# Performance work log

Hardware: AMD Instinct MI355X
Metric: run time of the kernel (lower is better)

Reference implementation:

```python
import jax, jax.numpy as jnp
import numpy as np

B, LQ, LK = 16, 1024, 2048
E, F, A = 512, 256, 512


def setup_inputs() -> dict:
    key = jax.random.key(0)
    ks = jax.random.split(key, 8)
    s_e = 1.0 / np.sqrt(E)
    s_f = 1.0 / np.sqrt(F)
    s_a = 1.0 / np.sqrt(A)
    return {
        "lstm_embeddings": jax.random.normal(ks[0], (B, LQ, E), jnp.float32),
        "optical_flow_features": jax.random.normal(ks[1], (B, LK, F), jnp.float32),
        "Wq": jax.random.normal(ks[2], (E, A), jnp.float32) * s_e,
        "bq": jnp.zeros((A,), jnp.float32),
        "Wk": jax.random.normal(ks[3], (F, A), jnp.float32) * s_f,
        "bk": jnp.zeros((A,), jnp.float32),
        "Wv": jax.random.normal(ks[4], (F, A), jnp.float32) * s_f,
        "bv": jnp.zeros((A,), jnp.float32),
        "Wo": jax.random.normal(ks[5], (A, E), jnp.float32) * s_a,
        "bo": jnp.zeros((E,), jnp.float32),
    }


def reference(lstm_embeddings, optical_flow_features, Wq, bq, Wk, bk, Wv, bv, Wo, bo):
    # Linear projections (x @ W + b), matching nn.Linear with W stored as [in, out]
    q = lstm_embeddings @ Wq + bq            # [B, LQ, A]
    k = optical_flow_features @ Wk + bk      # [B, LK, A]
    v = optical_flow_features @ Wv + bv      # [B, LK, A]
    # NOTE: original module does NOT scale scores by 1/sqrt(A) — stay faithful.
    scores = jnp.einsum("bqa,bka->bqk", q, k)      # [B, LQ, LK]
    weights = jax.nn.softmax(scores, axis=-1)
    context = jnp.einsum("bqk,bka->bqa", weights, v)  # [B, LQ, A]
    return context @ Wo + bo                          # [B, LQ, E]
```

## Files before the change

### kernel.cpp

```cpp
#include <hip/hip_runtime.h>


#define DEV static __device__ __forceinline__

typedef __attribute__((ext_vector_type(8))) short s8v;
typedef __attribute__((ext_vector_type(8))) _Float16 h8v;
typedef __attribute__((ext_vector_type(4))) _Float16 h4v;
typedef __attribute__((ext_vector_type(4))) float f4v;
typedef __attribute__((ext_vector_type(16))) float f16f;
typedef __attribute__((ext_vector_type(4))) float float4v;
typedef unsigned short u16;
typedef unsigned int u32;

constexpr int BB = 16;
constexpr int LQ = 1024;
constexpr int LK = 2048;
constexpr int E = 512;
constexpr int F = 256;

DEV u16 f2bf(float x) {
    u32 u = __builtin_bit_cast(u32, x);
    u += 0x7fff + ((u >> 16) & 1);
    return (u16)(u >> 16);
}
DEV float bf2f(u16 h) { return __builtin_bit_cast(float, (u32)h << 16); }

DEV f4v MF(s8v a, s8v b, f4v c) {
    return __builtin_amdgcn_mfma_f32_16x16x32_bf16(a, b, c, 0, 0, 0);
}
DEV f4v MF16(h8v a, h8v b, f4v c) {
    return __builtin_amdgcn_mfma_f32_16x16x32_f16(a, b, c, 0, 0, 0);
}
DEV f16f MF32(h8v a, h8v b, f16f c) {
    return __builtin_amdgcn_mfma_f32_32x32x16_f16(a, b, c, 0, 0, 0);
}

DEV void gll16(const _Float16* g, _Float16* l) {
    __builtin_amdgcn_global_load_lds(
        (const __attribute__((address_space(1))) u32*)g,
        (__attribute__((address_space(3))) u32*)l, 16, 0, 0);
}

__global__ __launch_bounds__(256) void prew(
    const float* __restrict__ y, _Float16* __restrict__ yA,
    _Float16* __restrict__ yB,
    const float* __restrict__ Wq, const float* __restrict__ bq,
    const float* __restrict__ Wk, const float* __restrict__ Wv,
    const float* __restrict__ bv, const float* __restrict__ Wo,
    const float* __restrict__ bo,
    u16* __restrict__ Mhb, u16* __restrict__ Ntb,
    float* __restrict__ wvec, float* __restrict__ cvec)
{
    __shared__ __align__(16) char smem[33536];
    const int tid = threadIdx.x;
    const int bi = blockIdx.x;

    if (bi < 1024) {
        float (*Y)[260] = (float(*)[260])smem;
        const int b = bi >> 6, t = bi & 63;
        const float* src = y + ((size_t)b * LK + t * 32) * F;
#pragma unroll
        for (int i = 0; i < 8; ++i) {
            int base = i * 1024 + tid * 4;
            int k = base >> 8, f = base & 255;
            *(float4v*)&Y[k][f] = *(const float4v*)(src + base);
        }
        __syncthreads();
        size_t tb = (size_t)(b * 64 + t) * 8192;
#pragma unroll
        for (int i = 0; i < 4; ++i) {
            int c = i * 256 + tid;
            int k = c & 31, hi = (c >> 5) & 1, fs = c >> 6;
            int f0 = fs * 16 + hi * 8;
            float4v v0 = *(const float4v*)&Y[k][f0];
            float4v v1 = *(const float4v*)&Y[k][f0 + 4];
            h8v v;
#pragma unroll
            for (int j = 0; j < 4; ++j) { v[j] = (_Float16)v0[j]; v[4 + j] = (_Float16)v1[j]; }
            *(h8v*)(yA + tb + (size_t)c * 8) = v;
        }
#pragma unroll
        for (int i = 0; i < 4; ++i) {
            int c = i * 256 + tid;
            int fl = c & 31, hi = (c >> 5) & 1, frag = c >> 6;
            int ft = frag >> 1, ks = frag & 1;
            int f = ft * 32 + fl, k0 = ks * 16 + hi * 8;
            h8v v;
#pragma unroll
            for (int j = 0; j < 8; ++j) v[j] = (_Float16)Y[k0 + j][f];
            *(h8v*)(yB + tb + (size_t)c * 8) = v;
        }
        return;
    }

    const int wb = bi - 1024;
    if (wb >= 64) {
        if (wb == 64) {
            const float* r = Wk + (size_t)tid * 512;
            float s = 0.f;
#pragma unroll 4
            for (int a = 0; a < 512; a += 4) {
                float4v v = *(const float4v*)(r + a);
                float4v bb = *(const float4v*)(bq + a);
                s += v[0] * bb[0] + v[1] * bb[1] + v[2] * bb[2] + v[3] * bb[3];
            }
            wvec[tid] = s;
        } else {
            int e = (wb - 65) * 256 + tid;
            float s = bo[e];
#pragma unroll 4
            for (int a = 0; a < 512; ++a) s += bv[a] * Wo[(size_t)a * 512 + e];
            cvec[e] = s;
        }
        return;
    }

    const bool ntm = wb >= 32;
    const int bj = ntm ? wb - 32 : wb;
    const int m0 = ntm ? (bj >> 2) * 64 : (bj >> 3) * 64;
    const int n0 = ntm ? (bj & 3) * 64 : (bj & 7) * 64;
    const float* Ag = ntm ? Wo : Wk;
    const float* Bg = ntm ? Wv : Wq;

    u16 (*Ash)[40] = (u16(*)[40])(smem);
    u16 (*Asl)[40] = (u16(*)[40])(smem + 5120);
    u16 (*Bsh)[40] = (u16(*)[40])(smem + 10240);
    u16 (*Bsl)[40] = (u16(*)[40])(smem + 15360);

    const int w = tid >> 6, lane = tid & 63;
    const int g = lane >> 4, qn = lane & 15;
    const int wr = w & 1, wc = w >> 1;

    f4v acc[2][2];
#pragma unroll
    for (int i = 0; i < 2; ++i)
#pragma unroll
        for (int j = 0; j < 2; ++j) acc[i][j] = (f4v){0.f, 0.f, 0.f, 0.f};

    for (int k0 = 0; k0 < 512; k0 += 32) {
        __syncthreads();
        if (!ntm) {
            int r = tid & 63, c = (tid >> 6) * 8;
            const float* s = Ag + (size_t)(m0 + r) * 512 + k0 + c;
            float4v v0 = *(const float4v*)s, v1 = *(const float4v*)(s + 4);
            short hh[8], ll[8];
#pragma unroll
            for (int i = 0; i < 8; ++i) {
                float x = (i < 4) ? v0[i] : v1[i - 4];
                u16 h = f2bf(x);
                hh[i] = (short)h;
                ll[i] = (short)f2bf(x - bf2f(h));
            }
            *(s8v*)&Ash[r][c] = (s8v){hh[0],hh[1],hh[2],hh[3],hh[4],hh[5],hh[6],hh[7]};
            *(s8v*)&Asl[r][c] = (s8v){ll[0],ll[1],ll[2],ll[3],ll[4],ll[5],ll[6],ll[7]};
        } else {
            int k = tid >> 3, mc = (tid & 7) * 8;
            const float* s = Ag + (size_t)(k0 + k) * 512 + m0 + mc;
            float4v v0 = *(const float4v*)s, v1 = *(const float4v*)(s + 4);
#pragma unroll
            for (int i = 0; i < 8; ++i) {
                float x = (i < 4) ? v0[i] : v1[i - 4];
                u16 h = f2bf(x);
                Ash[mc + i][k] = h;
                Asl[mc + i][k] = f2bf(x - bf2f(h));
            }
        }
        {
            int r = tid & 63, c = (tid >> 6) * 8;
            const float* s = Bg + (size_t)(n0 + r) * 512 + k0 + c;
            float4v v0 = *(const float4v*)s, v1 = *(const float4v*)(s + 4);
            short hh[8], ll[8];
#pragma unroll
            for (int i = 0; i < 8; ++i) {
                float x = (i < 4) ? v0[i] : v1[i - 4];
                u16 h = f2bf(x);
                hh[i] = (short)h;
                ll[i] = (short)f2bf(x - bf2f(h));
            }
            *(s8v*)&Bsh[r][c] = (s8v){hh[0],hh[1],hh[2],hh[3],hh[4],hh[5],hh[6],hh[7]};
            *(s8v*)&Bsl[r][c] = (s8v){ll[0],ll[1],ll[2],ll[3],ll[4],ll[5],ll[6],ll[7]};
        }
        __syncthreads();

        s8v ah[2], al[2], bh[2], bl[2];
#pragma unroll
        for (int mt = 0; mt < 2; ++mt) {
            ah[mt] = *(const s8v*)&Ash[wr * 32 + mt * 16 + qn][g * 8];
            al[mt] = *(const s8v*)&Asl[wr * 32 + mt * 16 + qn][g * 8];
        }
#pragma unroll
        for (int nt = 0; nt < 2; ++nt) {
            bh[nt] = *(const s8v*)&Bsh[wc * 32 + nt * 16 + qn][g * 8];
            bl[nt] = *(const s8v*)&Bsl[wc * 32 + nt * 16 + qn][g * 8];
        }
#pragma unroll
        for (int mt = 0; mt < 2; ++mt)
#pragma unroll
            for (int nt = 0; nt < 2; ++nt) {
                acc[mt][nt] = MF(ah[mt], bh[nt], acc[mt][nt]);
                acc[mt][nt] = MF(ah[mt], bl[nt], acc[mt][nt]);
                acc[mt][nt] = MF(al[mt], bh[nt], acc[mt][nt]);
            }
    }

#pragma unroll
    for (int mt = 0; mt < 2; ++mt)
#pragma unroll
        for (int nt = 0; nt < 2; ++nt)
#pragma unroll
            for (int r = 0; r < 4; ++r) {
                int gm = m0 + wr * 32 + mt * 16 + 4 * g + r;
                int gn = n0 + wc * 32 + nt * 16 + qn;
                float v = acc[mt][nt][r];
                if (!ntm) {
                    size_t off = (size_t)((gn >> 5) * 16 + (gm >> 4)) * 512 +
                                 (gm & 15) * 8 + ((gn >> 3) & 3) * 128 + (gn & 7);
                    Mhb[off] = __builtin_bit_cast(u16, (_Float16)v);
                } else {
                    size_t off = (size_t)((gn >> 5) * 32 + (gm >> 4)) * 512 +
                                 (gm & 15) * 8 + ((gn >> 3) & 3) * 128 + (gn & 7);
                    Ntb[off] = __builtin_bit_cast(u16, (_Float16)v);
                }
            }
}

__global__ __launch_bounds__(256) void qprime4(
    const float* __restrict__ x, const u16* __restrict__ Mhb,
    const float* __restrict__ wv, _Float16* __restrict__ q16)
{
    __shared__ _Float16 Xs[2][128][40];
    const int tid = threadIdx.x, w = tid >> 6, lane = tid & 63;
    const int g = lane >> 4, qn = lane & 15;
    const int m0 = blockIdx.x * 128;
    const int nh = blockIdx.y * 8;
    const int srow = tid >> 1, scol = (tid & 1) * 16;
    const _Float16* Mh = (const _Float16*)Mhb;

    f4v acc[2][8];
#pragma unroll
    for (int i = 0; i < 2; ++i)
#pragma unroll
        for (int j = 0; j < 8; ++j) acc[i][j] = (f4v){0.f, 0.f, 0.f, 0.f};

    float4v a0, a1, a2, a3;
    auto LDA = [&](int k0) {
        const float* s = x + (size_t)(m0 + srow) * 512 + k0 + scol;
        a0 = *(const float4v*)s;      a1 = *(const float4v*)(s + 4);
        a2 = *(const float4v*)(s + 8); a3 = *(const float4v*)(s + 12);
    };
    auto STA = [&](int buf) {
        h8v v0, v1;
#pragma unroll
        for (int j = 0; j < 4; ++j) {
            v0[j] = (_Float16)a0[j]; v0[4 + j] = (_Float16)a1[j];
            v1[j] = (_Float16)a2[j]; v1[4 + j] = (_Float16)a3[j];
        }
        *(h8v*)&Xs[buf][srow][scol] = v0;
        *(h8v*)&Xs[buf][srow][scol + 8] = v1;
    };

    LDA(0); STA(0); LDA(32);
    __syncthreads();

    for (int t = 0; t < 16; ++t) {
        const int cur = t & 1;
        h8v af[2];
#pragma unroll
        for (int mt = 0; mt < 2; ++mt)
            af[mt] = *(const h8v*)&Xs[cur][(w * 2 + mt) * 16 + qn][g * 8];
        const int fb = t * 16 + nh;
#pragma unroll
        for (int nt = 0; nt < 8; ++nt) {
            h8v bf = *(const h8v*)(Mh + (size_t)(fb + nt) * 512 + lane * 8);
            acc[0][nt] = MF16(af[0], bf, acc[0][nt]);
            acc[1][nt] = MF16(af[1], bf, acc[1][nt]);
        }
        if (t < 15) {
            STA(cur ^ 1);
            if (t < 14) LDA((t + 2) * 32);
            __syncthreads();
        }
    }

#pragma unroll
    for (int mt = 0; mt < 2; ++mt)
#pragma unroll
        for (int nt = 0; nt < 8; ++nt) {
            int col = (nh + nt) * 16 + qn;
            float wvc = wv[col];
#pragma unroll
            for (int r = 0; r < 4; ++r) {
                int row = m0 + w * 32 + mt * 16 + 4 * g + r;
                q16[(size_t)row * 256 + col] = (_Float16)(acc[mt][nt][r] + wvc);
            }
        }
}

__global__ __launch_bounds__(512) void flash5(
    const _Float16* __restrict__ q16, const _Float16* __restrict__ yA,
    const _Float16* __restrict__ yB, _Float16* __restrict__ part,
    float* __restrict__ ml)
{
    __shared__ _Float16 Asb[2][2][8192];
    __shared__ _Float16 Bsb[2][2][8192];
    __shared__ _Float16 Pls[8][1024];

    const int tid = threadIdx.x;
    const int w = tid >> 6, lane = tid & 63;
    const int q32 = lane & 31, hi = lane >> 5;

    int id = blockIdx.x;
    int xcd = id & 7, slot = id >> 3;
    int grp = xcd + 8 * (slot >> 2);
    int qb = slot & 3;
    int b = grp >> 2, z = grp & 3;
    const int qw = qb * 256 + w * 32;

    h8v qf[16];
    {
        const _Float16* qp = q16 + ((size_t)b * LQ + qw + q32) * 256 + hi * 8;
#pragma unroll
        for (int s = 0; s < 16; ++s) qf[s] = *(const h8v*)(qp + s * 16);
    }
    f16f ctx[8];
#pragma unroll
    for (int i = 0; i < 8; ++i) ctx[i] = (f16f){};
    float mrun = -3.0e38f, lrun = 0.f;

    const size_t tbe = (size_t)(b * 64 + z * 16) * 8192;

    auto STAGE = [&](int sup, int buf) {
#pragma unroll
        for (int j = 0; j < 2; ++j) {
            const _Float16* ga = yA + tbe + (size_t)(sup * 2 + j) * 8192 + tid * 8;
            const _Float16* gb = yB + tbe + (size_t)(sup * 2 + j) * 8192 + tid * 8;
            gll16(ga,        &Asb[buf][j][tid * 8]);
            gll16(ga + 4096, &Asb[buf][j][tid * 8 + 4096]);
            gll16(gb,        &Bsb[buf][j][tid * 8]);
            gll16(gb + 4096, &Bsb[buf][j][tid * 8 + 4096]);
        }
    };

    STAGE(0, 0);
    __syncthreads();

    int buf = 0;
    for (int s = 0; s < 8; ++s) {
        if (s < 7) STAGE(s + 1, buf ^ 1);
#pragma unroll
        for (int j = 0; j < 2; ++j) {
            const _Float16* Ap = &Asb[buf][j][0];
            const _Float16* Bp = &Bsb[buf][j][0];
            f16f S = (f16f){};
#pragma unroll
            for (int fs = 0; fs < 16; ++fs) {
                h8v a = *(const h8v*)(Ap + fs * 512 + lane * 8);
                S = MF32(a, qf[fs], S);
            }
            float mt = S[0];
#pragma unroll
            for (int r = 1; r < 16; ++r) mt = fmaxf(mt, S[r]);
            mt = fmaxf(mt, __shfl_xor(mt, 32));
            if (!__all(mt <= mrun + 8.f)) {
                float mnew = fmaxf(mrun, mt);
                float alpha = __expf(mrun - mnew);
                lrun *= alpha;
#pragma unroll
                for (int r = 0; r < 16; ++r) {
                    int qr = (r & 3) + 8 * (r >> 2) + 4 * hi;
                    float ar = __shfl(alpha, qr);
#pragma unroll
                    for (int ft = 0; ft < 8; ++ft) ctx[ft][r] *= ar;
                }
                mrun = mnew;
            }
            float p[16], ps = 0.f;
#pragma unroll
            for (int r = 0; r < 16; ++r) { p[r] = __expf(S[r] - mrun); ps += p[r]; }
            ps += __shfl_xor(ps, 32);
            lrun += ps;
            {
                _Float16* pw = &Pls[w][0];
#pragma unroll
                for (int r2 = 0; r2 < 4; ++r2) {
                    h4v pk = (h4v){(_Float16)p[4 * r2], (_Float16)p[4 * r2 + 1],
                                   (_Float16)p[4 * r2 + 2], (_Float16)p[4 * r2 + 3]};
                    *(h4v*)(pw + (r2 >> 1) * 512 + (r2 & 1) * 256 + q32 * 8 + hi * 4) = pk;
                }
            }
#pragma unroll
            for (int ks = 0; ks < 2; ++ks) {
                h8v pa = *(const h8v*)(&Pls[w][ks * 512] + lane * 8);
#pragma unroll
                for (int ft = 0; ft < 8; ++ft) {
                    h8v bf = *(const h8v*)(Bp + (ft * 2 + ks) * 512 + lane * 8);
                    ctx[ft] = MF32(pa, bf, ctx[ft]);
                }
            }
        }
        __syncthreads();
        buf ^= 1;
    }

    float linv = 1.f / lrun;
    _Float16* pp = part + ((size_t)z * (BB * LQ) + (size_t)b * LQ + qw) * 256;
#pragma unroll
    for (int r = 0; r < 16; ++r) {
        int qr = (r & 3) + 8 * (r >> 2) + 4 * hi;
        float ir = __shfl(linv, qr);
#pragma unroll
        for (int ft = 0; ft < 8; ++ft)
            pp[(size_t)qr * 256 + ft * 32 + q32] = (_Float16)(ctx[ft][r] * ir);
    }
    if (hi == 0) {
        size_t mi = (size_t)z * (BB * LQ) + (size_t)b * LQ + qw + q32;
        ml[2 * mi + 0] = mrun;
        ml[2 * mi + 1] = lrun;
    }
}

__global__ __launch_bounds__(256) void gemm2c(
    const _Float16* __restrict__ part, const float* __restrict__ ml,
    const u16* __restrict__ Ntb, const float* __restrict__ cvec,
    float* __restrict__ out)
{
    __shared__ _Float16 Asb[64][40];
    __shared__ float scl[64][4];
    const int tid = threadIdx.x;
    const int w = tid >> 6, lane = tid & 63;
    const int g = lane >> 4, qn = lane & 15;
    const int wr = w >> 1, wc = w & 1;
    const int m0 = blockIdx.x * 64, e0 = blockIdx.y * 256;
    constexpr size_t PL = (size_t)BB * LQ * F;
    constexpr size_t PR = (size_t)BB * LQ;

    if (tid < 64) {
        size_t i = m0 + tid;
        float m0v = ml[2 * i], l0v = ml[2 * i + 1];
        float m1v = ml[2 * (PR + i)], l1v = ml[2 * (PR + i) + 1];
        float m2v = ml[2 * (2 * PR + i)], l2v = ml[2 * (2 * PR + i) + 1];
        float m3v = ml[2 * (3 * PR + i)], l3v = ml[2 * (3 * PR + i) + 1];
        float M = fmaxf(fmaxf(m0v, m1v), fmaxf(m2v, m3v));
        float e0v = __expf(m0v - M), e1v = __expf(m1v - M);
        float e2v = __expf(m2v - M), e3v = __expf(m3v - M);
        float inv = 1.f / (l0v * e0v + l1v * e1v + l2v * e2v + l3v * e3v);
        scl[tid][0] = l0v * e0v * inv;
        scl[tid][1] = l1v * e1v * inv;
        scl[tid][2] = l2v * e2v * inv;
        scl[tid][3] = l3v * e3v * inv;
    }

    f4v acc[2][8];
#pragma unroll
    for (int i = 0; i < 2; ++i)
#pragma unroll
        for (int j = 0; j < 8; ++j) acc[i][j] = (f4v){0.f, 0.f, 0.f, 0.f};

    for (int k0 = 0; k0 < F; k0 += 32) {
        __syncthreads();
        {
            int r = tid & 63, c = (tid >> 6) * 8;
            size_t base = (size_t)(m0 + r) * F + k0 + c;
            h8v p0 = *(const h8v*)(part + base);
            h8v p1 = *(const h8v*)(part + PL + base);
            h8v p2 = *(const h8v*)(part + 2 * PL + base);
            h8v p3 = *(const h8v*)(part + 3 * PL + base);
            float s0 = scl[r][0], s1 = scl[r][1], s2 = scl[r][2], s3 = scl[r][3];
#pragma unroll
            for (int i = 0; i < 8; ++i) {
                float v = (float)p0[i] * s0 + (float)p1[i] * s1 +
                          (float)p2[i] * s2 + (float)p3[i] * s3;
                Asb[r][c + i] = (_Float16)v;
            }
        }
        __syncthreads();

        h8v ah[2], bh[8];
#pragma unroll
        for (int mt = 0; mt < 2; ++mt)
            ah[mt] = *(const h8v*)&Asb[wr * 32 + mt * 16 + qn][g * 8];
        int eb = (e0 + wc * 128) >> 4;
#pragma unroll
        for (int nt = 0; nt < 8; ++nt)
            bh[nt] = *(const h8v*)((const _Float16*)Ntb +
                     (size_t)((k0 >> 5) * 32 + eb + nt) * 512 + lane * 8);
#pragma unroll
        for (int mt = 0; mt < 2; ++mt)
#pragma unroll
            for (int nt = 0; nt < 8; ++nt)
                acc[mt][nt] = MF16(ah[mt], bh[nt], acc[mt][nt]);
    }

#pragma unroll
    for (int mt = 0; mt < 2; ++mt)
#pragma unroll
        for (int nt = 0; nt < 8; ++nt)
#pragma unroll
            for (int r = 0; r < 4; ++r) {
                int gm = m0 + wr * 32 + mt * 16 + 4 * g + r;
                int gn = e0 + wc * 128 + nt * 16 + qn;
                out[(size_t)gm * E + gn] = acc[mt][nt][r] + cvec[gn];
            }
}

extern "C" void kernel_launch(void* const* d_in, const int* in_sizes, int n_in,
                              void* d_out, int out_size, void* d_ws, size_t ws_size,
                              hipStream_t stream)
{
    const float* x  = (const float*)d_in[0];
    const float* y  = (const float*)d_in[1];
    const float* Wq = (const float*)d_in[2];
    const float* bq = (const float*)d_in[3];
    const float* Wk = (const float*)d_in[4];
    const float* Wv = (const float*)d_in[6];
    const float* bv = (const float*)d_in[7];
    const float* Wo = (const float*)d_in[8];
    const float* bo = (const float*)d_in[9];
    float* out = (float*)d_out;

    char* ws = (char*)d_ws;
    size_t off = 0;
    auto alloc = [&](size_t bytes) -> char* {
        char* p = ws + off;
        off = (off + bytes + 255) & ~(size_t)255;
        return p;
    };
    u16* Mhb  = (u16*)alloc(sizeof(u16) * F * E);
    float* wvec = (float*)alloc(sizeof(float) * F);
    float* cvec = (float*)alloc(sizeof(float) * E);
    u16* Ntb  = (u16*)alloc(sizeof(u16) * E * F);
    _Float16* q16 = (_Float16*)alloc(sizeof(u16) * (size_t)BB * LQ * F);
    _Float16* yA  = (_Float16*)alloc(sizeof(u16) * (size_t)BB * LK * F);
    _Float16* yB  = (_Float16*)alloc(sizeof(u16) * (size_t)BB * LK * F);
    _Float16* part = (_Float16*)alloc(sizeof(u16) * 4 * (size_t)BB * LQ * F);
    float* ml = (float*)alloc(sizeof(float) * 2 * 4 * (size_t)BB * LQ);
    (void)ws_size; (void)in_sizes; (void)n_in; (void)out_size;

    prew<<<dim3(1091), dim3(256), 0, stream>>>(
        y, yA, yB, Wq, bq, Wk, Wv, bv, Wo, bo, Mhb, Ntb, wvec, cvec);
    qprime4<<<dim3(BB * LQ / 128, 2), dim3(256), 0, stream>>>(x, Mhb, wvec, q16);
    flash5<<<dim3(256), dim3(512), 0, stream>>>(q16, yA, yB, part, ml);
    gemm2c<<<dim3(BB * LQ / 64, E / 256), dim3(256), 0, stream>>>(
        part, ml, Ntb, cvec, out);
}
```

Measured before the change: 137.3 us.

## Fold log2e into Q, use exp2, pass P via shuffles, halve qprime tile

The log2(e) factor is folded into the q16 projection so every softmax exponent becomes a native exp2, and the lazy-rescale threshold is adjusted to match. In the flash kernel the probability tile is no longer round-tripped through LDS: values are packed with cvt_pkrtz and exchanged between half-waves with shuffles to form the MFMA A operand directly. The score accumulation is split into two independent MFMA chains to shorten the dependency chain. Separately, the qprime kernel uses 64-row tiles instead of 128, doubling its grid, which gives more parallelism but less reuse of the weight loads.

```diff
diff --git a/kernel.cpp b/kernel.cpp
--- a/kernel.cpp
+++ b/kernel.cpp
@@ -5,10 +5,10 @@
 
 typedef __attribute__((ext_vector_type(8))) short s8v;
 typedef __attribute__((ext_vector_type(8))) _Float16 h8v;
-typedef __attribute__((ext_vector_type(4))) _Float16 h4v;
 typedef __attribute__((ext_vector_type(4))) float f4v;
 typedef __attribute__((ext_vector_type(16))) float f16f;
 typedef __attribute__((ext_vector_type(4))) float float4v;
+typedef __attribute__((ext_vector_type(4))) unsigned int u32x4;
 typedef unsigned short u16;
 typedef unsigned int u32;
 
@@ -33,6 +33,10 @@
 }
 DEV f16f MF32(h8v a, h8v b, f16f c) {
     return __builtin_amdgcn_mfma_f32_32x32x16_f16(a, b, c, 0, 0, 0);
+}
+DEV u32 pkh(float a, float b) {
+    auto t = __builtin_amdgcn_cvt_pkrtz(a, b);
+    return __builtin_bit_cast(u32, t);
 }
 
 DEV void gll16(const _Float16* g, _Float16* l) {
@@ -224,39 +228,33 @@
             }
 }
 
-__global__ __launch_bounds__(256) void qprime4(
+__global__ __launch_bounds__(256) void qprime5(
     const float* __restrict__ x, const u16* __restrict__ Mhb,
     const float* __restrict__ wv, _Float16* __restrict__ q16)
 {
-    __shared__ _Float16 Xs[2][128][40];
+    __shared__ _Float16 Xs[2][64][40];
     const int tid = threadIdx.x, w = tid >> 6, lane = tid & 63;
     const int g = lane >> 4, qn = lane & 15;
-    const int m0 = blockIdx.x * 128;
+    const int m0 = blockIdx.x * 64;
     const int nh = blockIdx.y * 8;
-    const int srow = tid >> 1, scol = (tid & 1) * 16;
+    const int srow = tid >> 2, scol = (tid & 3) * 8;
     const _Float16* Mh = (const _Float16*)Mhb;
 
-    f4v acc[2][8];
-#pragma unroll
-    for (int i = 0; i < 2; ++i)
-#pragma unroll
-        for (int j = 0; j < 8; ++j) acc[i][j] = (f4v){0.f, 0.f, 0.f, 0.f};
-
-    float4v a0, a1, a2, a3;
+    f4v acc[8];
+#pragma unroll
+    for (int n = 0; n < 8; ++n) acc[n] = (f4v){0.f, 0.f, 0.f, 0.f};
+
+    float4v a0, a1;
     auto LDA = [&](int k0) {
         const float* s = x + (size_t)(m0 + srow) * 512 + k0 + scol;
-        a0 = *(const float4v*)s;      a1 = *(const float4v*)(s + 4);
-        a2 = *(const float4v*)(s + 8); a3 = *(const float4v*)(s + 12);
+        a0 = *(const float4v*)s;
+        a1 = *(const float4v*)(s + 4);
     };
     auto STA = [&](int buf) {
-        h8v v0, v1;
-#pragma unroll
-        for (int j = 0; j < 4; ++j) {
-            v0[j] = (_Float16)a0[j]; v0[4 + j] = (_Float16)a1[j];
-            v1[j] = (_Float16)a2[j]; v1[4 + j] = (_Float16)a3[j];
-        }
-        *(h8v*)&Xs[buf][srow][scol] = v0;
-        *(h8v*)&Xs[buf][srow][scol + 8] = v1;
+        h8v v;
+#pragma unroll
+        for (int j = 0; j < 4; ++j) { v[j] = (_Float16)a0[j]; v[4 + j] = (_Float16)a1[j]; }
+        *(h8v*)&Xs[buf][srow][scol] = v;
     };
 
     LDA(0); STA(0); LDA(32);
@@ -264,16 +262,12 @@
 
     for (int t = 0; t < 16; ++t) {
         const int cur = t & 1;
-        h8v af[2];
-#pragma unroll
-        for (int mt = 0; mt < 2; ++mt)
-            af[mt] = *(const h8v*)&Xs[cur][(w * 2 + mt) * 16 + qn][g * 8];
+        h8v af = *(const h8v*)&Xs[cur][w * 16 + qn][g * 8];
         const int fb = t * 16 + nh;
 #pragma unroll
         for (int nt = 0; nt < 8; ++nt) {
             h8v bf = *(const h8v*)(Mh + (size_t)(fb + nt) * 512 + lane * 8);
-            acc[0][nt] = MF16(af[0], bf, acc[0][nt]);
-            acc[1][nt] = MF16(af[1], bf, acc[1][nt]);
+            acc[nt] = MF16(af, bf, acc[nt]);
         }
         if (t < 15) {
             STA(cur ^ 1);
@@ -283,38 +277,37 @@
     }
 
 #pragma unroll
-    for (int mt = 0; mt < 2; ++mt)
-#pragma unroll
-        for (int nt = 0; nt < 8; ++nt) {
-            int col = (nh + nt) * 16 + qn;
-            float wvc = wv[col];
-#pragma unroll
-            for (int r = 0; r < 4; ++r) {
-                int row = m0 + w * 32 + mt * 16 + 4 * g + r;
-                q16[(size_t)row * 256 + col] = (_Float16)(acc[mt][nt][r] + wvc);
-            }
-        }
-}
-
-__global__ __launch_bounds__(512) void flash5(
+    for (int nt = 0; nt < 8; ++nt) {
+        int col = (nh + nt) * 16 + qn;
+        float wvc = wv[col];
+#pragma unroll
+        for (int r = 0; r < 4; ++r) {
+            int row = m0 + w * 16 + 4 * g + r;
+            q16[(size_t)row * 256 + col] =
+                (_Float16)((acc[nt][r] + wvc) * 1.44269504f);
+        }
+    }
+}
+
+__global__ __launch_bounds__(512) void flash6(
     const _Float16* __restrict__ q16, const _Float16* __restrict__ yA,
     const _Float16* __restrict__ yB, _Float16* __restrict__ part,
     float* __restrict__ ml)
 {
     __shared__ _Float16 Asb[2][2][8192];
     __shared__ _Float16 Bsb[2][2][8192];
-    __shared__ _Float16 Pls[8][1024];
 
     const int tid = threadIdx.x;
-    const int w = tid >> 6, lane = tid & 63;
-    const int q32 = lane & 31, hi = lane >> 5;
+    const int lane = tid & 63;
+    const int q32 = lane & 31;
+    const int hi = lane >> 5;
 
     int id = blockIdx.x;
     int xcd = id & 7, slot = id >> 3;
     int grp = xcd + 8 * (slot >> 2);
     int qb = slot & 3;
     int b = grp >> 2, z = grp & 3;
-    const int qw = qb * 256 + w * 32;
+    const int qw = qb * 256 + (tid >> 6) * 32;
 
     h8v qf[16];
     {
@@ -351,19 +344,22 @@
         for (int j = 0; j < 2; ++j) {
             const _Float16* Ap = &Asb[buf][j][0];
             const _Float16* Bp = &Bsb[buf][j][0];
-            f16f S = (f16f){};
-#pragma unroll
-            for (int fs = 0; fs < 16; ++fs) {
-                h8v a = *(const h8v*)(Ap + fs * 512 + lane * 8);
-                S = MF32(a, qf[fs], S);
-            }
-            float mt = S[0];
-#pragma unroll
-            for (int r = 1; r < 16; ++r) mt = fmaxf(mt, S[r]);
+            f16f Sa = (f16f){}, Sb = (f16f){};
+#pragma unroll
+            for (int fs = 0; fs < 16; fs += 2) {
+                h8v a0 = *(const h8v*)(Ap + fs * 512 + lane * 8);
+                h8v a1 = *(const h8v*)(Ap + (fs + 1) * 512 + lane * 8);
+                Sa = MF32(a0, qf[fs], Sa);
+                Sb = MF32(a1, qf[fs + 1], Sb);
+            }
+            f16f S = Sa + Sb;
+            float mt = fmaxf(S[0], S[1]);
+#pragma unroll
+            for (int r = 2; r < 16; ++r) mt = fmaxf(mt, S[r]);
             mt = fmaxf(mt, __shfl_xor(mt, 32));
-            if (!__all(mt <= mrun + 8.f)) {
+            if (!__all(mt <= mrun + 11.5416f)) {
                 float mnew = fmaxf(mrun, mt);
-                float alpha = __expf(mrun - mnew);
+                float alpha = exp2f(mrun - mnew);
                 lrun *= alpha;
 #pragma unroll
                 for (int r = 0; r < 16; ++r) {
@@ -376,25 +372,33 @@
             }
             float p[16], ps = 0.f;
 #pragma unroll
-            for (int r = 0; r < 16; ++r) { p[r] = __expf(S[r] - mrun); ps += p[r]; }
+            for (int r = 0; r < 16; ++r) { p[r] = exp2f(S[r] - mrun); ps += p[r]; }
             ps += __shfl_xor(ps, 32);
             lrun += ps;
             {
-                _Float16* pw = &Pls[w][0];
-#pragma unroll
-                for (int r2 = 0; r2 < 4; ++r2) {
-                    h4v pk = (h4v){(_Float16)p[4 * r2], (_Float16)p[4 * r2 + 1],
-                                   (_Float16)p[4 * r2 + 2], (_Float16)p[4 * r2 + 3]};
-                    *(h4v*)(pw + (r2 >> 1) * 512 + (r2 & 1) * 256 + q32 * 8 + hi * 4) = pk;
+                u32 X0 = pkh(p[0], p[1]),   X1 = pkh(p[2], p[3]);
+                u32 Y0 = pkh(p[4], p[5]),   Y1 = pkh(p[6], p[7]);
+                u32 Z0 = pkh(p[8], p[9]),   Z1 = pkh(p[10], p[11]);
+                u32 W0 = pkh(p[12], p[13]), W1 = pkh(p[14], p[15]);
+                u32 M0 = hi ? X0 : Y0, M1 = hi ? X1 : Y1;
+                u32 N0 = hi ? Z0 : W0, N1 = hi ? Z1 : W1;
+                u32 sM0 = __shfl_xor(M0, 32), sM1 = __shfl_xor(M1, 32);
+                u32 sN0 = __shfl_xor(N0, 32), sN1 = __shfl_xor(N1, 32);
+                u32x4 A0u = (u32x4){hi ? sM0 : X0, hi ? sM1 : X1,
+                                    hi ? Y0 : sM0, hi ? Y1 : sM1};
+                u32x4 A1u = (u32x4){hi ? sN0 : Z0, hi ? sN1 : Z1,
+                                    hi ? W0 : sN0, hi ? W1 : sN1};
+                h8v pa0 = __builtin_bit_cast(h8v, A0u);
+                h8v pa1 = __builtin_bit_cast(h8v, A1u);
+#pragma unroll
+                for (int ft = 0; ft < 8; ++ft) {
+                    h8v bf = *(const h8v*)(Bp + (ft * 2 + 0) * 512 + lane * 8);
+                    ctx[ft] = MF32(pa0, bf, ctx[ft]);
                 }
-            }
-#pragma unroll
-            for (int ks = 0; ks < 2; ++ks) {
-                h8v pa = *(const h8v*)(&Pls[w][ks * 512] + lane * 8);
 #pragma unroll
                 for (int ft = 0; ft < 8; ++ft) {
-                    h8v bf = *(const h8v*)(Bp + (ft * 2 + ks) * 512 + lane * 8);
-                    ctx[ft] = MF32(pa, bf, ctx[ft]);
+                    h8v bf = *(const h8v*)(Bp + (ft * 2 + 1) * 512 + lane * 8);
+                    ctx[ft] = MF32(pa1, bf, ctx[ft]);
                 }
             }
         }
@@ -441,8 +445,8 @@
         float m2v = ml[2 * (2 * PR + i)], l2v = ml[2 * (2 * PR + i) + 1];
         float m3v = ml[2 * (3 * PR + i)], l3v = ml[2 * (3 * PR + i) + 1];
         float M = fmaxf(fmaxf(m0v, m1v), fmaxf(m2v, m3v));
-        float e0v = __expf(m0v - M), e1v = __expf(m1v - M);
-        float e2v = __expf(m2v - M), e3v = __expf(m3v - M);
+        float e0v = exp2f(m0v - M), e1v = exp2f(m1v - M);
+        float e2v = exp2f(m2v - M), e3v = exp2f(m3v - M);
         float inv = 1.f / (l0v * e0v + l1v * e1v + l2v * e2v + l3v * e3v);
         scl[tid][0] = l0v * e0v * inv;
         scl[tid][1] = l1v * e1v * inv;
@@ -538,8 +542,8 @@
 
     prew<<<dim3(1091), dim3(256), 0, stream>>>(
         y, yA, yB, Wq, bq, Wk, Wv, bv, Wo, bo, Mhb, Ntb, wvec, cvec);
-    qprime4<<<dim3(BB * LQ / 128, 2), dim3(256), 0, stream>>>(x, Mhb, wvec, q16);
-    flash5<<<dim3(256), dim3(512), 0, stream>>>(q16, yA, yB, part, ml);
+    qprime5<<<dim3(BB * LQ / 64, 2), dim3(256), 0, stream>>>(x, Mhb, wvec, q16);
+    flash6<<<dim3(256), dim3(512), 0, stream>>>(q16, yA, yB, part, ml);
     gemm2c<<<dim3(BB * LQ / 64, E / 256), dim3(256), 0, stream>>>(
         part, ml, Ntb, cvec, out);
 }
```

After: 137.2 us. Within noise of the previous version (-0.1%).

## Fold log2e into q, use exp2 in softmax, retile q-proj and output GEMMs

Applied to the files above, without the earlier changes.

The query projection now scales its output by log2(e), so the flash kernel and the combine step can use exp2f instead of __expf, and the rescale threshold is adjusted to match. The q-projection kernel is retiled to 64-row blocks, with double-buffered register prefetch of the B fragments across k steps. The output GEMM is retiled to 32-row blocks, each covering all 512 output columns. Together these aim to cut exponent arithmetic, hide global load latency and improve occupancy, at the cost of more blocks and more register pressure.

```diff
diff --git a/kernel.cpp b/kernel.cpp
--- a/kernel.cpp
+++ b/kernel.cpp
@@ -224,56 +224,62 @@
             }
 }
 
-__global__ __launch_bounds__(256) void qprime4(
+__global__ __launch_bounds__(256) void qprime6(
     const float* __restrict__ x, const u16* __restrict__ Mhb,
     const float* __restrict__ wv, _Float16* __restrict__ q16)
 {
-    __shared__ _Float16 Xs[2][128][40];
+    __shared__ _Float16 Xs[2][64][40];
     const int tid = threadIdx.x, w = tid >> 6, lane = tid & 63;
     const int g = lane >> 4, qn = lane & 15;
-    const int m0 = blockIdx.x * 128;
+    const int m0 = blockIdx.x * 64;
     const int nh = blockIdx.y * 8;
-    const int srow = tid >> 1, scol = (tid & 1) * 16;
+    const int srow = tid >> 2, scol = (tid & 3) * 8;
     const _Float16* Mh = (const _Float16*)Mhb;
 
-    f4v acc[2][8];
-#pragma unroll
-    for (int i = 0; i < 2; ++i)
-#pragma unroll
-        for (int j = 0; j < 8; ++j) acc[i][j] = (f4v){0.f, 0.f, 0.f, 0.f};
-
-    float4v a0, a1, a2, a3;
+    f4v acc[8];
+#pragma unroll
+    for (int n = 0; n < 8; ++n) acc[n] = (f4v){0.f, 0.f, 0.f, 0.f};
+
+    float4v a0, a1;
     auto LDA = [&](int k0) {
         const float* s = x + (size_t)(m0 + srow) * 512 + k0 + scol;
-        a0 = *(const float4v*)s;      a1 = *(const float4v*)(s + 4);
-        a2 = *(const float4v*)(s + 8); a3 = *(const float4v*)(s + 12);
+        a0 = *(const float4v*)s;
+        a1 = *(const float4v*)(s + 4);
     };
     auto STA = [&](int buf) {
-        h8v v0, v1;
-#pragma unroll
-        for (int j = 0; j < 4; ++j) {
-            v0[j] = (_Float16)a0[j]; v0[4 + j] = (_Float16)a1[j];
-            v1[j] = (_Float16)a2[j]; v1[4 + j] = (_Float16)a3[j];
-        }
-        *(h8v*)&Xs[buf][srow][scol] = v0;
-        *(h8v*)&Xs[buf][srow][scol + 8] = v1;
+        h8v v;
+#pragma unroll
+        for (int j = 0; j < 4; ++j) { v[j] = (_Float16)a0[j]; v[4 + j] = (_Float16)a1[j]; }
+        *(h8v*)&Xs[buf][srow][scol] = v;
     };
-
-    LDA(0); STA(0); LDA(32);
+    h8v b0[8], b1[8];
+    auto LDB0 = [&](int t) {
+        const int fb = t * 16 + nh;
+#pragma unroll
+        for (int nt = 0; nt < 8; ++nt)
+            b0[nt] = *(const h8v*)(Mh + (size_t)(fb + nt) * 512 + lane * 8);
+    };
+    auto LDB1 = [&](int t) {
+        const int fb = t * 16 + nh;
+#pragma unroll
+        for (int nt = 0; nt < 8; ++nt)
+            b1[nt] = *(const h8v*)(Mh + (size_t)(fb + nt) * 512 + lane * 8);
+    };
+
+    LDA(0); STA(0); LDA(32); LDB0(0);
     __syncthreads();
 
+#pragma unroll
     for (int t = 0; t < 16; ++t) {
         const int cur = t & 1;
-        h8v af[2];
-#pragma unroll
-        for (int mt = 0; mt < 2; ++mt)
-            af[mt] = *(const h8v*)&Xs[cur][(w * 2 + mt) * 16 + qn][g * 8];
-        const int fb = t * 16 + nh;
-#pragma unroll
-        for (int nt = 0; nt < 8; ++nt) {
-            h8v bf = *(const h8v*)(Mh + (size_t)(fb + nt) * 512 + lane * 8);
-            acc[0][nt] = MF16(af[0], bf, acc[0][nt]);
-            acc[1][nt] = MF16(af[1], bf, acc[1][nt]);
+        if (t < 15) { if (cur == 0) LDB1(t + 1); else LDB0(t + 1); }
+        h8v af = *(const h8v*)&Xs[cur][w * 16 + qn][g * 8];
+        if (cur == 0) {
+#pragma unroll
+            for (int nt = 0; nt < 8; ++nt) acc[nt] = MF16(af, b0[nt], acc[nt]);
+        } else {
+#pragma unroll
+            for (int nt = 0; nt < 8; ++nt) acc[nt] = MF16(af, b1[nt], acc[nt]);
         }
         if (t < 15) {
             STA(cur ^ 1);
@@ -283,20 +289,19 @@
     }
 
 #pragma unroll
-    for (int mt = 0; mt < 2; ++mt)
-#pragma unroll
-        for (int nt = 0; nt < 8; ++nt) {
-            int col = (nh + nt) * 16 + qn;
-            float wvc = wv[col];
-#pragma unroll
-            for (int r = 0; r < 4; ++r) {
-                int row = m0 + w * 32 + mt * 16 + 4 * g + r;
-                q16[(size_t)row * 256 + col] = (_Float16)(acc[mt][nt][r] + wvc);
-            }
-        }
-}
-
-__global__ __launch_bounds__(512) void flash5(
+    for (int nt = 0; nt < 8; ++nt) {
+        int col = (nh + nt) * 16 + qn;
+        float wvc = wv[col];
+#pragma unroll
+        for (int r = 0; r < 4; ++r) {
+            int row = m0 + w * 16 + 4 * g + r;
+            q16[(size_t)row * 256 + col] =
+                (_Float16)((acc[nt][r] + wvc) * 1.44269504f);
+        }
+    }
+}
+
+__global__ __launch_bounds__(512) void flash8(
     const _Float16* __restrict__ q16, const _Float16* __restrict__ yA,
     const _Float16* __restrict__ yB, _Float16* __restrict__ part,
     float* __restrict__ ml)
@@ -361,9 +366,9 @@
 #pragma unroll
             for (int r = 1; r < 16; ++r) mt = fmaxf(mt, S[r]);
             mt = fmaxf(mt, __shfl_xor(mt, 32));
-            if (!__all(mt <= mrun + 8.f)) {
+            if (!__all(mt <= mrun + 11.5416f)) {
                 float mnew = fmaxf(mrun, mt);
-                float alpha = __expf(mrun - mnew);
+                float alpha = exp2f(mrun - mnew);
                 lrun *= alpha;
 #pragma unroll
                 for (int r = 0; r < 16; ++r) {
@@ -376,7 +381,7 @@
             }
             float p[16], ps = 0.f;
 #pragma unroll
-            for (int r = 0; r < 16; ++r) { p[r] = __expf(S[r] - mrun); ps += p[r]; }
+            for (int r = 0; r < 16; ++r) { p[r] = exp2f(S[r] - mrun); ps += p[r]; }
             ps += __shfl_xor(ps, 32);
             lrun += ps;
             {
@@ -419,30 +424,29 @@
     }
 }
 
-__global__ __launch_bounds__(256) void gemm2c(
+__global__ __launch_bounds__(256) void gemm2c2(
     const _Float16* __restrict__ part, const float* __restrict__ ml,
     const u16* __restrict__ Ntb, const float* __restrict__ cvec,
     float* __restrict__ out)
 {
-    __shared__ _Float16 Asb[64][40];
-    __shared__ float scl[64][4];
+    __shared__ _Float16 Asb[32][40];
+    __shared__ float scl[32][4];
     const int tid = threadIdx.x;
     const int w = tid >> 6, lane = tid & 63;
     const int g = lane >> 4, qn = lane & 15;
-    const int wr = w >> 1, wc = w & 1;
-    const int m0 = blockIdx.x * 64, e0 = blockIdx.y * 256;
+    const int m0 = blockIdx.x * 32;
     constexpr size_t PL = (size_t)BB * LQ * F;
     constexpr size_t PR = (size_t)BB * LQ;
 
-    if (tid < 64) {
+    if (tid < 32) {
         size_t i = m0 + tid;
         float m0v = ml[2 * i], l0v = ml[2 * i + 1];
         float m1v = ml[2 * (PR + i)], l1v = ml[2 * (PR + i) + 1];
         float m2v = ml[2 * (2 * PR + i)], l2v = ml[2 * (2 * PR + i) + 1];
         float m3v = ml[2 * (3 * PR + i)], l3v = ml[2 * (3 * PR + i) + 1];
         float M = fmaxf(fmaxf(m0v, m1v), fmaxf(m2v, m3v));
-        float e0v = __expf(m0v - M), e1v = __expf(m1v - M);
-        float e2v = __expf(m2v - M), e3v = __expf(m3v - M);
+        float e0v = exp2f(m0v - M), e1v = exp2f(m1v - M);
+        float e2v = exp2f(m2v - M), e3v = exp2f(m3v - M);
         float inv = 1.f / (l0v * e0v + l1v * e1v + l2v * e2v + l3v * e3v);
         scl[tid][0] = l0v * e0v * inv;
         scl[tid][1] = l1v * e1v * inv;
@@ -459,46 +463,43 @@
     for (int k0 = 0; k0 < F; k0 += 32) {
         __syncthreads();
         {
-            int r = tid & 63, c = (tid >> 6) * 8;
-            size_t base = (size_t)(m0 + r) * F + k0 + c;
-            h8v p0 = *(const h8v*)(part + base);
-            h8v p1 = *(const h8v*)(part + PL + base);
-            h8v p2 = *(const h8v*)(part + 2 * PL + base);
-            h8v p3 = *(const h8v*)(part + 3 * PL + base);
+            int r = tid >> 3, cc = (tid & 7) * 4;
+            size_t base = (size_t)(m0 + r) * F + k0 + cc;
+            h4v p0 = *(const h4v*)(part + base);
+            h4v p1 = *(const h4v*)(part + PL + base);
+            h4v p2 = *(const h4v*)(part + 2 * PL + base);
+            h4v p3 = *(const h4v*)(part + 3 * PL + base);
             float s0 = scl[r][0], s1 = scl[r][1], s2 = scl[r][2], s3 = scl[r][3];
 #pragma unroll
-            for (int i = 0; i < 8; ++i) {
+            for (int i = 0; i < 4; ++i) {
                 float v = (float)p0[i] * s0 + (float)p1[i] * s1 +
                           (float)p2[i] * s2 + (float)p3[i] * s3;
-                Asb[r][c + i] = (_Float16)v;
+                Asb[r][cc + i] = (_Float16)v;
             }
         }
         __syncthreads();
 
-        h8v ah[2], bh[8];
+        h8v ah[2];
 #pragma unroll
         for (int mt = 0; mt < 2; ++mt)
-            ah[mt] = *(const h8v*)&Asb[wr * 32 + mt * 16 + qn][g * 8];
-        int eb = (e0 + wc * 128) >> 4;
+            ah[mt] = *(const h8v*)&Asb[mt * 16 + qn][g * 8];
+#pragma unroll
+        for (int nt = 0; nt < 8; ++nt) {
+            h8v bh = *(const h8v*)((const _Float16*)Ntb +
+                     (size_t)((k0 >> 5) * 32 + w * 8 + nt) * 512 + lane * 8);
+            acc[0][nt] = MF16(ah[0], bh, acc[0][nt]);
+            acc[1][nt] = MF16(ah[1], bh, acc[1][nt]);
+        }
+    }
+
+#pragma unroll
+    for (int mt = 0; mt < 2; ++mt)
 #pragma unroll
         for (int nt = 0; nt < 8; ++nt)
-            bh[nt] = *(const h8v*)((const _Float16*)Ntb +
-                     (size_t)((k0 >> 5) * 32 + eb + nt) * 512 + lane * 8);
-#pragma unroll
-        for (int mt = 0; mt < 2; ++mt)
-#pragma unroll
-            for (int nt = 0; nt < 8; ++nt)
-                acc[mt][nt] = MF16(ah[mt], bh[nt], acc[mt][nt]);
-    }
-
-#pragma unroll
-    for (int mt = 0; mt < 2; ++mt)
-#pragma unroll
-        for (int nt = 0; nt < 8; ++nt)
 #pragma unroll
             for (int r = 0; r < 4; ++r) {
-                int gm = m0 + wr * 32 + mt * 16 + 4 * g + r;
-                int gn = e0 + wc * 128 + nt * 16 + qn;
+                int gm = m0 + mt * 16 + 4 * g + r;
+                int gn = w * 128 + nt * 16 + qn;
                 out[(size_t)gm * E + gn] = acc[mt][nt][r] + cvec[gn];
             }
 }
@@ -538,8 +539,8 @@
 
     prew<<<dim3(1091), dim3(256), 0, stream>>>(
         y, yA, yB, Wq, bq, Wk, Wv, bv, Wo, bo, Mhb, Ntb, wvec, cvec);
-    qprime4<<<dim3(BB * LQ / 128, 2), dim3(256), 0, stream>>>(x, Mhb, wvec, q16);
-    flash5<<<dim3(256), dim3(512), 0, stream>>>(q16, yA, yB, part, ml);
-    gemm2c<<<dim3(BB * LQ / 64, E / 256), dim3(256), 0, stream>>>(
+    qprime6<<<dim3(BB * LQ / 64, 2), dim3(256), 0, stream>>>(x, Mhb, wvec, q16);
+    flash8<<<dim3(256), dim3(512), 0, stream>>>(q16, yA, yB, part, ml);
+    gemm2c2<<<dim3(BB * LQ / 32), dim3(256), 0, stream>>>(
         part, ml, Ntb, cvec, out);
 }
```

New measurement: 135.7 us. About the same (-1.2%).
